# Performance work log

Hardware: AMD Instinct MI355X
Metric: run time of the kernel (lower is better)

The kernel has to match this reference:

```python
import jax, jax.numpy as jnp
import numpy as np

SL, BS, HS, FFN = 2048, 1, 512, 2048
E, TOP_K = 8, 2


def setup_inputs() -> dict:
    key = jax.random.key(0)
    k_x, k_w, k_i, k_w1, k_w2 = jax.random.split(key, 5)
    x = jax.random.normal(k_x, (SL, BS, HS), dtype=jnp.float32)
    expert_weights = jax.random.uniform(k_w, (SL * BS, TOP_K), dtype=jnp.float32)
    expert_indices = jax.random.randint(k_i, (SL * BS, TOP_K), 0, E, dtype=jnp.int32)
    # grouped expert MLP params (megablocks GroupedMLP, regular type, no bias)
    w1 = jax.random.normal(k_w1, (E, HS, FFN), dtype=jnp.float32) * (HS ** -0.5)
    w2 = jax.random.normal(k_w2, (E, FFN, HS), dtype=jnp.float32) * (FFN ** -0.5)
    return {"x": x, "expert_weights": expert_weights, "expert_indices": expert_indices,
            "w1": w1, "w2": w2}


def reference(x, expert_weights, expert_indices, w1, w2):
    sl, bs, hs = x.shape
    n_tok = sl * bs
    xf = x.reshape(n_tok, hs)                      # [N, hs]
    ew = expert_weights.reshape(-1)                # [N*top_k]
    ei = expert_indices.reshape(-1)                # [N*top_k]

    # indices_and_bins: stable radix sort of assignments by expert id
    indices = jnp.argsort(ei)                      # stable in jax -> sorted assignment ids
    bin_ids = ei[indices]                          # sorted expert id per assignment

    # megablocks gather: row for assignment i is indices[i] // top_k
    rows = indices // TOP_K                        # [T]
    xg = xf[rows]                                  # [T, hs] expert-contiguous tokens

    # grouped GEMM expert MLP (dense masked loop over fixed expert count)
    outg = jnp.zeros_like(xg)
    for e in range(E):
        m = (bin_ids == e).astype(x.dtype)[:, None]
        h = jax.nn.gelu(xg @ w1[e], approximate=False)   # [T, ffn]
        outg = outg + m * (h @ w2[e])                    # [T, hs]

    # buffer.index_add_(0, E*input_indices + bin_ids, output.detach())
    buf_idx = E * rows + bin_ids
    buffer = jnp.zeros((n_tok * E, hs), x.dtype).at[buf_idx].add(
        jax.lax.stop_gradient(outg))

    # megablocks scatter: weighted combine back to token order
    y = jnp.zeros((n_tok, hs), x.dtype).at[rows].add(outg * ew[indices][:, None])
    return y.reshape(sl, bs, hs), buffer.reshape(n_tok, E, hs)
```

## Files before the change

kernel.cpp:

```cpp
#include <hip/hip_runtime.h>
#include <hip/hip_bf16.h>

#define NTOK 2048
#define TOPK 2
#define HS   512
#define FFN  2048
#define NE   8
#define TASSIGN (NTOK*TOPK)
#define PAD  5120
#define MAXT128 40
#define MAXT64  72

typedef __attribute__((ext_vector_type(8))) short bf16x8;
typedef __attribute__((ext_vector_type(4))) float f32x4;

static const size_t OFF_XBF  = 0;
static const size_t OFF_W1T  = 2097152;
static const size_t OFF_W2T  = 18874368;
static const size_t OFF_H    = 35651584;
static const size_t OFF_OUTV = 56623104;
static const size_t OFF_RT   = 77594624;
static const size_t OFF_HROF = 77615104;
static const size_t OFF_TE128= 77631488;
static const size_t OFF_TR128= 77631648;
static const size_t OFF_TE64 = 77631808;
static const size_t OFF_TR64 = 77632096;

__device__ __forceinline__ unsigned short f2bf(float f) {
    union { __hip_bfloat16 h; unsigned short u; } v;
    v.h = __float2bfloat16(f);
    return v.u;
}

__device__ __forceinline__ int swz(int r, int byte_off) {
    return byte_off ^ ((r & 7) << 4);
}

#define GLOAD16(gsrc, ldst) \
    __builtin_amdgcn_global_load_lds((const __attribute__((address_space(1))) void*)(gsrc), \
                                     (__attribute__((address_space(3))) void*)(ldst), 16, 0, 0)

__device__ __forceinline__ void dev_transpose(const float* __restrict__ in,
                                              unsigned short* __restrict__ out,
                                              int R, int C, int e, int rb, int cb, int tid) {
    __shared__ unsigned short t[32][33];
    int tx = tid & 31, ty = tid >> 5;
    const float* ip = in + (size_t)e * R * C;
    unsigned short* op = out + (size_t)e * C * R;
#pragma unroll
    for (int i = 0; i < 4; i++) {
        int r = ty + i * 8;
        t[r][tx] = f2bf(ip[(size_t)(rb + r) * C + cb + tx]);
    }
    __syncthreads();
#pragma unroll
    for (int i = 0; i < 4; i++) {
        int c = ty + i * 8;
        op[(size_t)(cb + c) * R + rb + tx] = t[tx][c];
    }
}

__global__ __launch_bounds__(256) void k_prep(
        const float* __restrict__ x, const float* __restrict__ w1,
        const float* __restrict__ w2, const int* __restrict__ ei,
        unsigned short* __restrict__ xbf, unsigned short* __restrict__ w1T,
        unsigned short* __restrict__ w2T,
        int* __restrict__ rowtok, int* __restrict__ hrof,
        int* __restrict__ te128, int* __restrict__ tr128,
        int* __restrict__ te64, int* __restrict__ tr64) {
    int b = blockIdx.x;
    int tid = threadIdx.x;
    if (b == 0) {
        __shared__ int cnt[NE], offpad[NE], cur[NE];
        for (int i = tid; i < PAD; i += 256) rowtok[i] = 0;
        if (tid < NE) cnt[tid] = 0;
        __syncthreads();
        for (int a = tid; a < TASSIGN; a += 256) atomicAdd(&cnt[ei[a]], 1);
        __syncthreads();
        if (tid == 0) {
            int o = 0, t1 = 0, t2 = 0;
            for (int e = 0; e < NE; e++) {
                offpad[e] = o; cur[e] = 0;
                for (int r = 0; r < cnt[e]; r += 128) { te128[t1] = e; tr128[t1] = o + r; t1++; }
                for (int r = 0; r < cnt[e]; r += 64)  { te64[t2]  = e; tr64[t2]  = o + r; t2++; }
                o += (cnt[e] + 127) / 128 * 128;
            }
            for (; t1 < MAXT128; t1++) te128[t1] = -1;
            for (; t2 < MAXT64;  t2++) te64[t2]  = -1;
        }
        __syncthreads();
        for (int a = tid; a < TASSIGN; a += 256) {
            int e = ei[a];
            int r = atomicAdd(&cur[e], 1);
            int hr = offpad[e] + r;
            rowtok[hr] = a >> 1;
            hrof[a] = hr;
        }
    } else if (b < 1 + 1024) {
        int i = ((b - 1) * 256 + tid) * 4;
        float4 v = *(const float4*)(x + i);
        ushort4 o;
        o.x = f2bf(v.x); o.y = f2bf(v.y); o.z = f2bf(v.z); o.w = f2bf(v.w);
        *(ushort4*)(xbf + i) = o;
    } else if (b < 1 + 1024 + 8192) {
        int blk = b - 1025;
        int e = blk >> 10, rem = blk & 1023;
        dev_transpose(w1, w1T, HS, FFN, e, (rem >> 6) * 32, (rem & 63) * 32, tid);
    } else {
        int blk = b - 9217;
        int e = blk >> 10, rem = blk & 1023;
        dev_transpose(w2, w2T, FFN, HS, e, (rem >> 4) * 32, (rem & 15) * 32, tid);
    }
}

template<int BM, int BN, int KFULL, int KLOC, bool G1>
__global__ __launch_bounds__(256) void k_gemm(
        const unsigned short* __restrict__ A,
        const unsigned short* __restrict__ B,
        void* __restrict__ outp,
        const int* __restrict__ rowtok,
        const int* __restrict__ te, const int* __restrict__ tr, int N) {
    constexpr int MI = BM / 32, NJ = BN / 32;
    constexpr int PA = BM / 32, PB = BN / 32;
    constexpr int ABYTES = BM * 64 * 2, BBYTES = BN * 64 * 2;
    constexpr int NSTEP = KLOC / 64;
    static_assert(NSTEP % 2 == 0, "even steps");

    int mt = blockIdx.y;
    int e = te[mt];
    if (e < 0) return;
    int hr0 = tr[mt];
    int ct = blockIdx.x;
    int kz = blockIdx.z;
    int k0 = kz * KLOC;

    __shared__ int4 ldsv[(2 * (ABYTES + BBYTES)) / 16];
    char* A0 = (char*)ldsv;
    char* A1 = A0 + ABYTES;
    char* B0 = A1 + ABYTES;
    char* B1 = B0 + BBYTES;

    int tid = threadIdx.x;
    int lane = tid & 63, wave = tid >> 6;
    int wm = wave >> 1, wn = wave & 1;

    const char* asrc[PA];
    const char* bsrc[PB];
    int adoff[PA], bdoff[PB];
#pragma unroll
    for (int p = 0; p < PA; p++) {
        int idx = p * 256 + tid;
        int r = idx >> 3, c8 = idx & 7;
        int c8s = c8 ^ (r & 7);
        size_t row = G1 ? (size_t)rowtok[hr0 + r] : (size_t)(hr0 + r);
        asrc[p] = (const char*)(A + row * KFULL + k0) + c8s * 16;
        adoff[p] = (p * 256 + wave * 64) * 16;
    }
#pragma unroll
    for (int p = 0; p < PB; p++) {
        int idx = p * 256 + tid;
        int r = idx >> 3, c8 = idx & 7;
        int c8s = c8 ^ (r & 7);
        bsrc[p] = (const char*)(B + ((size_t)e * N + (size_t)ct * BN + r) * KFULL + k0) + c8s * 16;
        bdoff[p] = (p * 256 + wave * 64) * 16;
    }

    f32x4 acc[MI][NJ] = {};

    auto stage = [&](char* Ad, char* Bd, int s) {
        int kb = s * 128;
#pragma unroll
        for (int p = 0; p < PA; p++) GLOAD16(asrc[p] + kb, Ad + adoff[p]);
#pragma unroll
        for (int p = 0; p < PB; p++) GLOAD16(bsrc[p] + kb, Bd + bdoff[p]);
    };
    auto compute = [&](const char* As, const char* Bs) {
#pragma unroll
        for (int kk = 0; kk < 64; kk += 32) {
            bf16x8 af[MI], bfv[NJ];
#pragma unroll
            for (int i = 0; i < MI; i++) {
                int ar = wm * (BM / 2) + i * 16 + (lane & 15);
                af[i] = *(const bf16x8*)(As + swz(ar, ar * 128 + kk * 2 + (lane >> 4) * 16));
            }
#pragma unroll
            for (int j = 0; j < NJ; j++) {
                int bc = wn * (BN / 2) + j * 16 + (lane & 15);
                bfv[j] = *(const bf16x8*)(Bs + swz(bc, bc * 128 + kk * 2 + (lane >> 4) * 16));
            }
#pragma unroll
            for (int i = 0; i < MI; i++)
#pragma unroll
                for (int j = 0; j < NJ; j++)
                    acc[i][j] = __builtin_amdgcn_mfma_f32_16x16x32_bf16(af[i], bfv[j], acc[i][j], 0, 0, 0);
        }
    };

    stage(A0, B0, 0);
    __syncthreads();
#pragma unroll 1
    for (int s = 0; s < NSTEP; s += 2) {
        if (s + 1 < NSTEP) stage(A1, B1, s + 1);
        compute(A0, B0);
        __syncthreads();
        if (s + 2 < NSTEP) stage(A0, B0, s + 2);
        compute(A1, B1);
        __syncthreads();
    }

    if constexpr (G1) {
        unsigned short* O = (unsigned short*)outp;
#pragma unroll
        for (int i = 0; i < MI; i++)
#pragma unroll
            for (int j = 0; j < NJ; j++)
#pragma unroll
                for (int q = 0; q < 4; q++) {
                    int row = hr0 + wm * (BM / 2) + i * 16 + (lane >> 4) * 4 + q;
                    int col = ct * BN + wn * (BN / 2) + j * 16 + (lane & 15);
                    float v = acc[i][j][q];
                    float g = 0.5f * v * (1.0f + erff(v * 0.70710678118f));
                    O[(size_t)row * N + col] = f2bf(g);
                }
    } else {
        float* O = (float*)outp + (size_t)kz * PAD * HS;
#pragma unroll
        for (int i = 0; i < MI; i++)
#pragma unroll
            for (int j = 0; j < NJ; j++)
#pragma unroll
                for (int q = 0; q < 4; q++) {
                    int row = hr0 + wm * (BM / 2) + i * 16 + (lane >> 4) * 4 + q;
                    int col = ct * BN + wn * (BN / 2) + j * 16 + (lane & 15);
                    O[(size_t)row * N + col] = acc[i][j][q];
                }
    }
}

__global__ __launch_bounds__(256) void k_combine(
        const float4* __restrict__ outv, const int* __restrict__ ei,
        const float* __restrict__ ew, const int* __restrict__ hrof,
        float4* __restrict__ y, float4* __restrict__ buf) {
    constexpr int SPLIT_OFF = PAD * HS / 4;
    int g = blockIdx.x * 256 + threadIdx.x;
    int t = g >> 7, c4 = g & 127;
    int a0 = 2 * t, a1 = a0 + 1;
    int h0 = hrof[a0], h1 = hrof[a1];
    float4 p0a = outv[(size_t)h0 * (HS / 4) + c4];
    float4 p0b = outv[SPLIT_OFF + (size_t)h0 * (HS / 4) + c4];
    float4 p1a = outv[(size_t)h1 * (HS / 4) + c4];
    float4 p1b = outv[SPLIT_OFF + (size_t)h1 * (HS / 4) + c4];
    float4 o0 = make_float4(p0a.x + p0b.x, p0a.y + p0b.y, p0a.z + p0b.z, p0a.w + p0b.w);
    float4 o1 = make_float4(p1a.x + p1b.x, p1a.y + p1b.y, p1a.z + p1b.z, p1a.w + p1b.w);
    float w0 = ew[a0], w1 = ew[a1];
    y[g] = make_float4(w0 * o0.x + w1 * o1.x, w0 * o0.y + w1 * o1.y,
                       w0 * o0.z + w1 * o1.z, w0 * o0.w + w1 * o1.w);
    int e0 = ei[a0], e1 = ei[a1];
    size_t base = (size_t)t * (NE * HS / 4) + c4;
#pragma unroll
    for (int e = 0; e < NE; e++) {
        float4 v = make_float4(0.f, 0.f, 0.f, 0.f);
        if (e == e0) { v.x += o0.x; v.y += o0.y; v.z += o0.z; v.w += o0.w; }
        if (e == e1) { v.x += o1.x; v.y += o1.y; v.z += o1.z; v.w += o1.w; }
        buf[base + (size_t)e * (HS / 4)] = v;
    }
}

extern "C" void kernel_launch(void* const* d_in, const int* in_sizes, int n_in,
                              void* d_out, int out_size, void* d_ws, size_t ws_size,
                              hipStream_t stream) {
    const float* x  = (const float*)d_in[0];
    const float* ew = (const float*)d_in[1];
    const int*   ei = (const int*)d_in[2];
    const float* w1 = (const float*)d_in[3];
    const float* w2 = (const float*)d_in[4];

    char* ws = (char*)d_ws;
    unsigned short* xbf  = (unsigned short*)(ws + OFF_XBF);
    unsigned short* w1T  = (unsigned short*)(ws + OFF_W1T);
    unsigned short* w2T  = (unsigned short*)(ws + OFF_W2T);
    unsigned short* Hb   = (unsigned short*)(ws + OFF_H);
    float*          outv = (float*)(ws + OFF_OUTV);
    int*            rowtok = (int*)(ws + OFF_RT);
    int*            hrof   = (int*)(ws + OFF_HROF);
    int*            te128  = (int*)(ws + OFF_TE128);
    int*            tr128  = (int*)(ws + OFF_TR128);
    int*            te64   = (int*)(ws + OFF_TE64);
    int*            tr64   = (int*)(ws + OFF_TR64);

    float* y   = (float*)d_out;
    float* buf = (float*)d_out + (size_t)NTOK * HS;

    k_prep<<<1 + 1024 + 8192 + 8192, 256, 0, stream>>>(
        x, w1, w2, ei, xbf, w1T, w2T, rowtok, hrof, te128, tr128, te64, tr64);
    k_gemm<128, 128, HS, HS, true><<<dim3(FFN / 128, MAXT128), 256, 0, stream>>>(
        xbf, w1T, Hb, rowtok, te128, tr128, FFN);
    k_gemm<64, 64, FFN, FFN / 2, false><<<dim3(HS / 64, MAXT64, 2), 256, 0, stream>>>(
        Hb, w2T, outv, rowtok, te64, tr64, HS);
    k_combine<<<NTOK * HS / 4 / 256, 256, 0, stream>>>(
        (const float4*)outv, ei, ew, hrof, (float4*)y, (float4*)buf);
}
```

Baseline: 101.2 us.

## Overlap w2 transpose with first grouped GEMM and coarsen transpose blocks

Moves the w2 fp32-to-bf16 transpose out of the prep kernel and into extra blocks of the first GEMM launch, so that conversion runs alongside the GEMM1 tiles. Each transpose block now handles a strip of 16 32x32 tiles instead of one tile, which cuts the block count and launch overhead. GEMM1 tiles change from 128x128 to 128x64 with a 1D grid, which gives more blocks. The cost is extra LDS use and mixed block types in one launch, which may hurt occupancy or balance.

```diff
diff --git a/kernel.cpp b/kernel.cpp
--- a/kernel.cpp
+++ b/kernel.cpp
@@ -40,34 +40,39 @@
     __builtin_amdgcn_global_load_lds((const __attribute__((address_space(1))) void*)(gsrc), \
                                      (__attribute__((address_space(3))) void*)(ldst), 16, 0, 0)
 
-__device__ __forceinline__ void dev_transpose(const float* __restrict__ in,
-                                              unsigned short* __restrict__ out,
-                                              int R, int C, int e, int rb, int cb, int tid) {
-    __shared__ unsigned short t[32][33];
+__device__ __forceinline__ void tr_strip(const float* __restrict__ in,
+                                         unsigned short* __restrict__ out,
+                                         int R, int C, int e, int rb, int cb0, int ncb,
+                                         int tid, unsigned short* t) {
     int tx = tid & 31, ty = tid >> 5;
     const float* ip = in + (size_t)e * R * C;
     unsigned short* op = out + (size_t)e * C * R;
-#pragma unroll
-    for (int i = 0; i < 4; i++) {
-        int r = ty + i * 8;
-        t[r][tx] = f2bf(ip[(size_t)(rb + r) * C + cb + tx]);
-    }
-    __syncthreads();
-#pragma unroll
-    for (int i = 0; i < 4; i++) {
-        int c = ty + i * 8;
-        op[(size_t)(cb + c) * R + rb + tx] = t[tx][c];
-    }
-}
-
-__global__ __launch_bounds__(256) void k_prep(
+#pragma unroll 1
+    for (int it = 0; it < ncb; ++it) {
+        int cb = (cb0 + it) * 32;
+        __syncthreads();
+#pragma unroll
+        for (int i = 0; i < 4; i++) {
+            int r = ty + i * 8;
+            t[r * 33 + tx] = f2bf(ip[(size_t)(rb + r) * C + cb + tx]);
+        }
+        __syncthreads();
+#pragma unroll
+        for (int i = 0; i < 4; i++) {
+            int c = ty + i * 8;
+            op[(size_t)(cb + c) * R + rb + tx] = t[tx * 33 + c];
+        }
+    }
+}
+
+__global__ __launch_bounds__(256) void k_prep1(
         const float* __restrict__ x, const float* __restrict__ w1,
-        const float* __restrict__ w2, const int* __restrict__ ei,
+        const int* __restrict__ ei,
         unsigned short* __restrict__ xbf, unsigned short* __restrict__ w1T,
-        unsigned short* __restrict__ w2T,
         int* __restrict__ rowtok, int* __restrict__ hrof,
         int* __restrict__ te128, int* __restrict__ tr128,
         int* __restrict__ te64, int* __restrict__ tr64) {
+    __shared__ unsigned short tsh[32 * 33];
     int b = blockIdx.x;
     int tid = threadIdx.x;
     if (b == 0) {
@@ -102,23 +107,135 @@
         ushort4 o;
         o.x = f2bf(v.x); o.y = f2bf(v.y); o.z = f2bf(v.z); o.w = f2bf(v.w);
         *(ushort4*)(xbf + i) = o;
-    } else if (b < 1 + 1024 + 8192) {
+    } else {
         int blk = b - 1025;
-        int e = blk >> 10, rem = blk & 1023;
-        dev_transpose(w1, w1T, HS, FFN, e, (rem >> 6) * 32, (rem & 63) * 32, tid);
-    } else {
-        int blk = b - 9217;
-        int e = blk >> 10, rem = blk & 1023;
-        dev_transpose(w2, w2T, FFN, HS, e, (rem >> 4) * 32, (rem & 15) * 32, tid);
-    }
-}
-
-template<int BM, int BN, int KFULL, int KLOC, bool G1>
-__global__ __launch_bounds__(256) void k_gemm(
+        int e = blk >> 6, rem = blk & 63;
+        int rbt = rem >> 2, q = rem & 3;
+        tr_strip(w1, w1T, HS, FFN, e, rbt * 32, q * 16, 16, tid, tsh);
+    }
+}
+
+__global__ __launch_bounds__(256) void k_g1w2t(
         const unsigned short* __restrict__ A,
         const unsigned short* __restrict__ B,
-        void* __restrict__ outp,
+        unsigned short* __restrict__ Hout,
         const int* __restrict__ rowtok,
+        const int* __restrict__ te, const int* __restrict__ tr,
+        const float* __restrict__ w2, unsigned short* __restrict__ w2T) {
+    __shared__ int4 smem4[49152 / 16];
+    int b = blockIdx.x;
+    int tid = threadIdx.x;
+
+    if (b >= 1280) {
+        int blk = b - 1280;
+        int e = blk >> 6, rbt = blk & 63;
+        tr_strip(w2, w2T, FFN, HS, e, rbt * 32, 0, 16, tid, (unsigned short*)smem4);
+        return;
+    }
+
+    constexpr int BM = 128, BN = 64, K = HS;
+    constexpr int MI = 4, NJ = 2, PA = 4, PB = 2;
+    constexpr int ABYTES = BM * 64 * 2, BBYTES = BN * 64 * 2;
+    constexpr int NSTEP = K / 64;
+    constexpr int N = FFN;
+
+    int ct = b & 31;
+    int mt = b >> 5;
+    int e = te[mt];
+    if (e < 0) return;
+    int hr0 = tr[mt];
+
+    char* A0 = (char*)smem4;
+    char* A1 = A0 + ABYTES;
+    char* B0 = A1 + ABYTES;
+    char* B1 = B0 + BBYTES;
+
+    int lane = tid & 63, wave = tid >> 6;
+    int wm = wave >> 1, wn = wave & 1;
+
+    const char* asrc[PA];
+    const char* bsrc[PB];
+    int adoff[PA], bdoff[PB];
+#pragma unroll
+    for (int p = 0; p < PA; p++) {
+        int idx = p * 256 + tid;
+        int r = idx >> 3, c8 = idx & 7;
+        int c8s = c8 ^ (r & 7);
+        size_t row = (size_t)rowtok[hr0 + r];
+        asrc[p] = (const char*)(A + row * K) + c8s * 16;
+        adoff[p] = (p * 256 + wave * 64) * 16;
+    }
+#pragma unroll
+    for (int p = 0; p < PB; p++) {
+        int idx = p * 256 + tid;
+        int r = idx >> 3, c8 = idx & 7;
+        int c8s = c8 ^ (r & 7);
+        bsrc[p] = (const char*)(B + ((size_t)e * N + (size_t)ct * BN + r) * K) + c8s * 16;
+        bdoff[p] = (p * 256 + wave * 64) * 16;
+    }
+
+    f32x4 acc[MI][NJ] = {};
+
+    auto stage = [&](char* Ad, char* Bd, int s) {
+        int kb = s * 128;
+#pragma unroll
+        for (int p = 0; p < PA; p++) GLOAD16(asrc[p] + kb, Ad + adoff[p]);
+#pragma unroll
+        for (int p = 0; p < PB; p++) GLOAD16(bsrc[p] + kb, Bd + bdoff[p]);
+    };
+    auto compute = [&](const char* As, const char* Bs) {
+#pragma unroll
+        for (int kk = 0; kk < 64; kk += 32) {
+            bf16x8 af[MI], bfv[NJ];
+#pragma unroll
+            for (int i = 0; i < MI; i++) {
+                int ar = wm * (BM / 2) + i * 16 + (lane & 15);
+                af[i] = *(const bf16x8*)(As + swz(ar, ar * 128 + kk * 2 + (lane >> 4) * 16));
+            }
+#pragma unroll
+            for (int j = 0; j < NJ; j++) {
+                int bc = wn * (BN / 2) + j * 16 + (lane & 15);
+                bfv[j] = *(const bf16x8*)(Bs + swz(bc, bc * 128 + kk * 2 + (lane >> 4) * 16));
+            }
+#pragma unroll
+            for (int i = 0; i < MI; i++)
+#pragma unroll
+                for (int j = 0; j < NJ; j++)
+                    acc[i][j] = __builtin_amdgcn_mfma_f32_16x16x32_bf16(af[i], bfv[j], acc[i][j], 0, 0, 0);
+        }
+    };
+
+    stage(A0, B0, 0);
+    __syncthreads();
+#pragma unroll 1
+    for (int s = 0; s < NSTEP; s += 2) {
+        if (s + 1 < NSTEP) stage(A1, B1, s + 1);
+        compute(A0, B0);
+        __syncthreads();
+        if (s + 2 < NSTEP) stage(A0, B0, s + 2);
+        compute(A1, B1);
+        __syncthreads();
+    }
+
+#pragma unroll
+    for (int i = 0; i < MI; i++)
+#pragma unroll
+        for (int j = 0; j < NJ; j++)
+#pragma unroll
+            for (int q = 0; q < 4; q++) {
+                int row = hr0 + wm * (BM / 2) + i * 16 + (lane >> 4) * 4 + q;
+                int col = ct * BN + wn * (BN / 2) + j * 16 + (lane & 15);
+                float v = acc[i][j][q];
+                float g = 0.5f * v * (1.0f + erff(v * 0.70710678118f));
+                Hout[(size_t)row * N + col] = f2bf(g);
+            }
+}
+
+template<int BM, int BN, int KFULL, int KLOC>
+__global__ __launch_bounds__(256) void k_gemm2(
+        const unsigned short* __restrict__ A,
+        const unsigned short* __restrict__ B,
+        float* __restrict__ outp,
         const int* __restrict__ te, const int* __restrict__ tr, int N) {
     constexpr int MI = BM / 32, NJ = BN / 32;
     constexpr int PA = BM / 32, PB = BN / 32;
@@ -152,8 +269,7 @@
         int idx = p * 256 + tid;
         int r = idx >> 3, c8 = idx & 7;
         int c8s = c8 ^ (r & 7);
-        size_t row = G1 ? (size_t)rowtok[hr0 + r] : (size_t)(hr0 + r);
-        asrc[p] = (const char*)(A + row * KFULL + k0) + c8s * 16;
+        asrc[p] = (const char*)(A + (size_t)(hr0 + r) * KFULL + k0) + c8s * 16;
         adoff[p] = (p * 256 + wave * 64) * 16;
     }
 #pragma unroll
@@ -208,33 +324,17 @@
         __syncthreads();
     }
 
-    if constexpr (G1) {
-        unsigned short* O = (unsigned short*)outp;
-#pragma unroll
-        for (int i = 0; i < MI; i++)
-#pragma unroll
-            for (int j = 0; j < NJ; j++)
-#pragma unroll
-                for (int q = 0; q < 4; q++) {
-                    int row = hr0 + wm * (BM / 2) + i * 16 + (lane >> 4) * 4 + q;
-                    int col = ct * BN + wn * (BN / 2) + j * 16 + (lane & 15);
-                    float v = acc[i][j][q];
-                    float g = 0.5f * v * (1.0f + erff(v * 0.70710678118f));
-                    O[(size_t)row * N + col] = f2bf(g);
-                }
-    } else {
-        float* O = (float*)outp + (size_t)kz * PAD * HS;
-#pragma unroll
-        for (int i = 0; i < MI; i++)
-#pragma unroll
-            for (int j = 0; j < NJ; j++)
-#pragma unroll
-                for (int q = 0; q < 4; q++) {
-                    int row = hr0 + wm * (BM / 2) + i * 16 + (lane >> 4) * 4 + q;
-                    int col = ct * BN + wn * (BN / 2) + j * 16 + (lane & 15);
-                    O[(size_t)row * N + col] = acc[i][j][q];
-                }
-    }
+    float* O = outp + (size_t)kz * PAD * HS;
+#pragma unroll
+    for (int i = 0; i < MI; i++)
+#pragma unroll
+        for (int j = 0; j < NJ; j++)
+#pragma unroll
+            for (int q = 0; q < 4; q++) {
+                int row = hr0 + wm * (BM / 2) + i * 16 + (lane >> 4) * 4 + q;
+                int col = ct * BN + wn * (BN / 2) + j * 16 + (lane & 15);
+                O[(size_t)row * N + col] = acc[i][j][q];
+            }
 }
 
 __global__ __launch_bounds__(256) void k_combine(
@@ -291,12 +391,12 @@
     float* y   = (float*)d_out;
     float* buf = (float*)d_out + (size_t)NTOK * HS;
 
-    k_prep<<<1 + 1024 + 8192 + 8192, 256, 0, stream>>>(
-        x, w1, w2, ei, xbf, w1T, w2T, rowtok, hrof, te128, tr128, te64, tr64);
-    k_gemm<128, 128, HS, HS, true><<<dim3(FFN / 128, MAXT128), 256, 0, stream>>>(
-        xbf, w1T, Hb, rowtok, te128, tr128, FFN);
-    k_gemm<64, 64, FFN, FFN / 2, false><<<dim3(HS / 64, MAXT64, 2), 256, 0, stream>>>(
-        Hb, w2T, outv, rowtok, te64, tr64, HS);
+    k_prep1<<<1537, 256, 0, stream>>>(
+        x, w1, ei, xbf, w1T, rowtok, hrof, te128, tr128, te64, tr64);
+    k_g1w2t<<<1792, 256, 0, stream>>>(
+        xbf, w1T, Hb, rowtok, te128, tr128, w2, w2T);
+    k_gemm2<64, 64, FFN, FFN / 2><<<dim3(HS / 64, MAXT64, 2), 256, 0, stream>>>(
+        Hb, w2T, outv, te64, tr64, HS);
     k_combine<<<NTOK * HS / 4 / 256, 256, 0, stream>>>(
         (const float4*)outv, ei, ew, hrof, (float4*)y, (float4*)buf);
 }
```

Measured after the change: 95.00 us. 1.06x faster.
